# Kernel tuning notes

Hardware: AMD Instinct MI355X
Metric: run time of the kernel (lower is better)

Reference implementation:

```python
import jax, jax.numpy as jnp
import numpy as np

LN_EPS = 1e-5


def mlp_block(x, W, b, g, beta):
    # Linear -> LayerNorm -> ReLU  (MLP_Block)
    h = x @ W.T + b
    mu = jnp.mean(h, axis=-1, keepdims=True)
    var = jnp.mean((h - mu) ** 2, axis=-1, keepdims=True)
    h = (h - mu) / jnp.sqrt(var + LN_EPS) * g + beta
    return jax.nn.relu(h)


def interaction(a, bfeat, gW, gb, gg, gbt, pW, pb, pg, pbt, awg, abg, awp, abp):
    # Interaction_Estimator.forward(a, bfeat)
    g_align = mlp_block(a, gW, gb, gg, gbt)       # [B,L,D]
    p_align = mlp_block(bfeat, pW, pb, pg, pbt)    # [B,L,D]
    # atten[b,l,i,j] = g_align[b,l,i] * p_align[b,l,j]
    # geno_att[b,l,i] = sigmoid(sum_j atten[b,l,i,j]*awg[j] + abg)
    #               = sigmoid(g_align[b,l,i] * (p_align[b,l,:]\cdot awg) + abg)
    geno_att = jax.nn.sigmoid(g_align * jnp.einsum('bld,d->bl', p_align, awg)[..., None] + abg)
    # path_att[b,l,j] = sigmoid(sum_i atten[b,l,i,j]*awp[i] + abp)
    path_att = jax.nn.sigmoid(p_align * jnp.einsum('bld,d->bl', g_align, awp)[..., None] + abp)
    return p_align * path_att + g_align * geno_att


def setup_inputs() -> dict:
    B, L, D = 128, 16, 256
    key = jax.random.key(0)
    ks = iter(jax.random.split(key, 64))
    inp = {
        'gfeat': jax.random.normal(next(ks), (B, L, D), jnp.float32),
        'pfeat': jax.random.normal(next(ks), (B, L, D), jnp.float32),
    }

    def mlp_params(prefix):
        inp[prefix + '_W'] = jax.random.normal(next(ks), (D, D), jnp.float32) * 0.05
        inp[prefix + '_b'] = jnp.zeros((D,), jnp.float32)
        inp[prefix + '_g'] = jnp.ones((D,), jnp.float32)
        inp[prefix + '_beta'] = jnp.zeros((D,), jnp.float32)

    def atten_params(prefix):
        inp[prefix + 'w'] = jax.random.normal(next(ks), (D,), jnp.float32) * 0.05
        inp[prefix + 'b'] = jnp.zeros((), jnp.float32)

    mlp_params('gs')  # geno_spec
    mlp_params('ps')  # path_spec
    mlp_params('c_g'); mlp_params('c_p'); atten_params('c_ag'); atten_params('c_ap')  # common
    mlp_params('s_g'); mlp_params('s_p'); atten_params('s_ag'); atten_params('s_ap')  # synergy
    return inp


def reference(gfeat, pfeat,
              gs_W, gs_b, gs_g, gs_beta,
              ps_W, ps_b, ps_g, ps_beta,
              c_g_W, c_g_b, c_g_g, c_g_beta, c_p_W, c_p_b, c_p_g, c_p_beta, c_agw, c_agb, c_apw, c_apb,
              s_g_W, s_g_b, s_g_g, s_g_beta, s_p_W, s_p_b, s_p_g, s_p_beta, s_agw, s_agb, s_apw, s_apb):
    g_spec = mlp_block(gfeat, gs_W, gs_b, gs_g, gs_beta)
    p_spec = mlp_block(pfeat, ps_W, ps_b, ps_g, ps_beta)
    # NOTE: original calls encoder(pfeat, gfeat) (args swapped) -- kept faithful.
    common = interaction(pfeat, gfeat, c_g_W, c_g_b, c_g_g, c_g_beta,
                         c_p_W, c_p_b, c_p_g, c_p_beta, c_agw, c_agb, c_apw, c_apb)
    synergy = interaction(pfeat, gfeat, s_g_W, s_g_b, s_g_g, s_g_beta,
                          s_p_W, s_p_b, s_p_g, s_p_beta, s_agw, s_agb, s_apw, s_apb)
    return (common, synergy, g_spec, p_spec)
```

## Files before the change

### kernel.cpp

```cpp
#include <hip/hip_runtime.h>

typedef __attribute__((ext_vector_type(8))) short bf16x8;
typedef __attribute__((ext_vector_type(4))) float f32x4;
typedef unsigned short u16;
typedef unsigned int u32;

__device__ __forceinline__ u16 f2bf(float f) {
    u32 u = __builtin_bit_cast(u32, f);
    return (u16)((u + 0x7FFFu + ((u >> 16) & 1u)) >> 16);
}
__device__ __forceinline__ float sigm(float x) { return 1.f / (1.f + __expf(-x)); }
__device__ __forceinline__ float red16(float x) {
    x += __shfl_xor(x, 1, 64);
    x += __shfl_xor(x, 2, 64);
    x += __shfl_xor(x, 4, 64);
    x += __shfl_xor(x, 8, 64);
    return x;
}
__device__ __forceinline__ uint4 pack8(const float* s) {
    f32x4 v0 = *(const f32x4*)s;
    f32x4 v1 = *(const f32x4*)(s + 4);
    uint4 o;
    o.x = (u32)f2bf(v0.x) | ((u32)f2bf(v0.y) << 16);
    o.y = (u32)f2bf(v0.z) | ((u32)f2bf(v0.w) << 16);
    o.z = (u32)f2bf(v1.x) | ((u32)f2bf(v1.y) << 16);
    o.w = (u32)f2bf(v1.z) | ((u32)f2bf(v1.w) << 16);
    return o;
}

struct PrepArgs { const float* W[6]; const float* xg; const float* xp; u16* wf; u16* xf; };

__global__ __launch_bounds__(256) void prep_kernel(PrepArgs a) {
    int gid = blockIdx.x * 256 + threadIdx.x;
    if (gid < 49152) {
        int l = gid & 63, kk = (gid >> 6) & 7, nt = (gid >> 9) & 3,
            w = (gid >> 11) & 3, mlp = gid >> 13;
        int n = w * 64 + nt * 16 + (l & 15);
        int k0 = kk * 32 + (l >> 4) * 8;
        *(uint4*)(a.wf + (size_t)gid * 8) = pack8(a.W[mlp] + n * 256 + k0);
    } else if (gid < 49152 + 131072) {
        int r = gid - 49152;
        const float* x = (r >> 16) ? a.xp : a.xg;
        int q = r & 65535;
        int l = q & 63, kk = (q >> 6) & 7, mt = q >> 9;
        int row = mt * 16 + (l & 15);
        int k0 = kk * 32 + (l >> 4) * 8;
        *(uint4*)(a.xf + (size_t)r * 8) = pack8(x + row * 256 + k0);
    }
}

struct PairTask {
    const u16 *xfG, *xfP;
    const u16 *WG, *WP;
    const float *bG, *gmG, *beG;
    const float *bP, *gmP, *beP;
    const float *awG, *awP;
    const float *attbP, *attbG;
    float *outG, *outP;
    int interact;
};
struct FusedArgs { PairTask p[3]; };

__global__ __launch_bounds__(256) void fused_kernel(FusedArgs args) {
    __shared__ float red_s[2][16][4];
    __shared__ float red_q[2][16][4];
    __shared__ float red_d[2][16][4];

    int wg = blockIdx.x;
    int swz = (wg & 7) * 48 + (wg >> 3);
    int pair = swz >> 7;
    int mt = swz & 127;
    PairTask tk = args.p[pair];

    int tid = threadIdx.x;
    int wave = tid >> 6;
    int lane = tid & 63;
    int cq = lane & 15, rq = lane >> 4;

    float bb[2][4], gm[2][4], be[2][4], aw[2][4];
#pragma unroll
    for (int g = 0; g < 2; ++g)
#pragma unroll
        for (int nt = 0; nt < 4; ++nt) {
            int c = wave * 64 + nt * 16 + cq;
            bb[g][nt] = g ? tk.bP[c] : tk.bG[c];
            gm[g][nt] = g ? tk.gmP[c] : tk.gmG[c];
            be[g][nt] = g ? tk.beP[c] : tk.beG[c];
            aw[g][nt] = tk.interact ? (g ? tk.awP[c] : tk.awG[c]) : 0.f;
        }
    float battP = tk.interact ? *tk.attbP : 0.f;
    float battG = tk.interact ? *tk.attbG : 0.f;

    bf16x8 aF[2][8];
#pragma unroll
    for (int kk = 0; kk < 8; ++kk) {
        aF[0][kk] = *(const bf16x8*)(tk.xfG + ((size_t)(mt * 8 + kk) * 64 + lane) * 8);
        aF[1][kk] = *(const bf16x8*)(tk.xfP + ((size_t)(mt * 8 + kk) * 64 + lane) * 8);
    }

    f32x4 acc[2][4];
#pragma unroll
    for (int g = 0; g < 2; ++g)
#pragma unroll
        for (int nt = 0; nt < 4; ++nt) acc[g][nt] = (f32x4){0.f, 0.f, 0.f, 0.f};

    const u16* wb0 = tk.WG + (size_t)wave * 16384 + lane * 8;
    const u16* wb1 = tk.WP + (size_t)wave * 16384 + lane * 8;

#pragma unroll
    for (int kk = 0; kk < 8; ++kk) {
#pragma unroll
        for (int nt = 0; nt < 4; ++nt) {
            bf16x8 b0 = *(const bf16x8*)(wb0 + (size_t)(nt * 8 + kk) * 512);
            acc[0][nt] = __builtin_amdgcn_mfma_f32_16x16x32_bf16(aF[0][kk], b0, acc[0][nt], 0, 0, 0);
            bf16x8 b1 = *(const bf16x8*)(wb1 + (size_t)(nt * 8 + kk) * 512);
            acc[1][nt] = __builtin_amdgcn_mfma_f32_16x16x32_bf16(aF[1][kk], b1, acc[1][nt], 0, 0, 0);
        }
    }

    float v[2][4][4];
#pragma unroll
    for (int r = 0; r < 4; ++r) {
#pragma unroll
        for (int g = 0; g < 2; ++g) {
            float s = 0.f, q = 0.f;
#pragma unroll
            for (int nt = 0; nt < 4; ++nt) {
                float t = acc[g][nt][r] + bb[g][nt];
                v[g][nt][r] = t;
                s += t; q += t * t;
            }
            s = red16(s); q = red16(q);
            if (cq == 0) {
                red_s[g][rq * 4 + r][wave] = s;
                red_q[g][rq * 4 + r][wave] = q;
            }
        }
    }
    __syncthreads();

    float o[2][4][4];
#pragma unroll
    for (int r = 0; r < 4; ++r) {
        int row = rq * 4 + r;
#pragma unroll
        for (int g = 0; g < 2; ++g) {
            f32x4 s4 = *(const f32x4*)&red_s[g][row][0];
            f32x4 q4 = *(const f32x4*)&red_q[g][row][0];
            float s = s4.x + s4.y + s4.z + s4.w;
            float q = q4.x + q4.y + q4.z + q4.w;
            float mean = s * (1.f / 256.f);
            float var = q * (1.f / 256.f) - mean * mean;
            float rstd = rsqrtf(var + 1e-5f);
#pragma unroll
            for (int nt = 0; nt < 4; ++nt)
                o[g][nt][r] = fmaxf((v[g][nt][r] - mean) * rstd * gm[g][nt] + be[g][nt], 0.f);
        }
    }

    if (!tk.interact) {
#pragma unroll
        for (int r = 0; r < 4; ++r) {
            int grow = mt * 16 + rq * 4 + r;
#pragma unroll
            for (int nt = 0; nt < 4; ++nt) {
                int c = wave * 64 + nt * 16 + cq;
                tk.outG[(size_t)grow * 256 + c] = o[0][nt][r];
                tk.outP[(size_t)grow * 256 + c] = o[1][nt][r];
            }
        }
    } else {
#pragma unroll
        for (int r = 0; r < 4; ++r) {
            float dg = 0.f, dp = 0.f;
#pragma unroll
            for (int nt = 0; nt < 4; ++nt) {
                dg += o[0][nt][r] * aw[0][nt];
                dp += o[1][nt][r] * aw[1][nt];
            }
            dg = red16(dg); dp = red16(dp);
            if (cq == 0) {
                red_d[0][rq * 4 + r][wave] = dg;
                red_d[1][rq * 4 + r][wave] = dp;
            }
        }
        __syncthreads();
#pragma unroll
        for (int r = 0; r < 4; ++r) {
            int row = rq * 4 + r;
            f32x4 d4 = *(const f32x4*)&red_d[0][row][0];
            f32x4 e4 = *(const f32x4*)&red_d[1][row][0];
            float dG = d4.x + d4.y + d4.z + d4.w;
            float dP = e4.x + e4.y + e4.z + e4.w;
            int grow = mt * 16 + row;
#pragma unroll
            for (int nt = 0; nt < 4; ++nt) {
                int c = wave * 64 + nt * 16 + cq;
                float og = o[0][nt][r], op = o[1][nt][r];
                tk.outG[(size_t)grow * 256 + c] =
                    op * sigm(op * dG + battP) + og * sigm(og * dP + battG);
            }
        }
    }
}

extern "C" void kernel_launch(void* const* d_in, const int* in_sizes, int n_in,
                              void* d_out, int out_size, void* d_ws, size_t ws_size,
                              hipStream_t stream) {
    const float* gfeat = (const float*)d_in[0];
    const float* pfeat = (const float*)d_in[1];
    float* out = (float*)d_out;
    const size_t S = (size_t)2048 * 256;

    float* out_common = out + 0 * S;
    float* out_syn    = out + 1 * S;
    float* out_gspec  = out + 2 * S;
    float* out_pspec  = out + 3 * S;

    u16* wf = (u16*)d_ws;
    u16* xf = wf + 6 * 65536;
    u16* xf_g = xf;
    u16* xf_p = xf + 524288;

    PrepArgs pa;
    pa.W[0] = (const float*)d_in[2];
    pa.W[1] = (const float*)d_in[6];
    pa.W[2] = (const float*)d_in[10];
    pa.W[3] = (const float*)d_in[14];
    pa.W[4] = (const float*)d_in[22];
    pa.W[5] = (const float*)d_in[26];
    pa.xg = gfeat; pa.xp = pfeat;
    pa.wf = wf; pa.xf = xf;
    hipLaunchKernelGGL(prep_kernel, dim3(704), dim3(256), 0, stream, pa);

    FusedArgs fa;
    fa.p[0] = { xf_g, xf_p, wf + 0 * 65536, wf + 1 * 65536,
                (const float*)d_in[3], (const float*)d_in[4], (const float*)d_in[5],
                (const float*)d_in[7], (const float*)d_in[8], (const float*)d_in[9],
                nullptr, nullptr, nullptr, nullptr,
                out_gspec, out_pspec, 0 };
    fa.p[1] = { xf_p, xf_g, wf + 2 * 65536, wf + 3 * 65536,
                (const float*)d_in[11], (const float*)d_in[12], (const float*)d_in[13],
                (const float*)d_in[15], (const float*)d_in[16], (const float*)d_in[17],
                (const float*)d_in[20] , (const float*)d_in[18] ,
                (const float*)d_in[21] , (const float*)d_in[19] ,
                out_common, nullptr, 1 };
    fa.p[2] = { xf_p, xf_g, wf + 4 * 65536, wf + 5 * 65536,
                (const float*)d_in[23], (const float*)d_in[24], (const float*)d_in[25],
                (const float*)d_in[27], (const float*)d_in[28], (const float*)d_in[29],
                (const float*)d_in[32] , (const float*)d_in[30] ,
                (const float*)d_in[33] , (const float*)d_in[31] ,
                out_syn, nullptr, 1 };

    hipLaunchKernelGGL(fused_kernel, dim3(384), dim3(256), 0, stream, fa);
}
```

Baseline: 23.32 us.

## Replicate packed weights per XCD and software-pipeline loads in fused GEMM

The prep kernel now writes up to eight copies of the packed bf16 weights, one per XCD group (selected by wg&7), so each chiplet's blocks read weights from their own copy and hit their local L2 instead of contending across chiplets. The fused kernel no longer preloads all A fragments up front. It issues A and B fragment loads two K-steps ahead in a three-stage register ring, so memory latency overlaps the MFMA work. It also adds a launch-bounds occupancy hint of two blocks per SM. The cost is more prep work (eight times the weight conversion writes) and higher register pressure from the buffered fragments.

```diff
diff --git a/kernel.cpp b/kernel.cpp
--- a/kernel.cpp
+++ b/kernel.cpp
@@ -28,18 +28,25 @@
     return o;
 }
 
-struct PrepArgs { const float* W[6]; const float* xg; const float* xp; u16* wf; u16* xf; };
+struct PrepArgs {
+    const float* W[6]; const float* xg; const float* xp;
+    u16* wf; u16* xf; int nrep;
+};
 
 __global__ __launch_bounds__(256) void prep_kernel(PrepArgs a) {
-    int gid = blockIdx.x * 256 + threadIdx.x;
-    if (gid < 49152) {
+    int blk = blockIdx.x, tid = threadIdx.x;
+    int wblk = 192 * a.nrep;
+    if (blk < wblk) {
+        int rep = (a.nrep == 8) ? (blk & 7) : 0;
+        int gid = ((a.nrep == 8) ? (blk >> 3) : blk) * 256 + tid;
         int l = gid & 63, kk = (gid >> 6) & 7, nt = (gid >> 9) & 3,
             w = (gid >> 11) & 3, mlp = gid >> 13;
         int n = w * 64 + nt * 16 + (l & 15);
         int k0 = kk * 32 + (l >> 4) * 8;
-        *(uint4*)(a.wf + (size_t)gid * 8) = pack8(a.W[mlp] + n * 256 + k0);
-    } else if (gid < 49152 + 131072) {
-        int r = gid - 49152;
+        *(uint4*)(a.wf + ((size_t)rep * 49152 + gid) * 8) =
+            pack8(a.W[mlp] + n * 256 + k0);
+    } else {
+        int r = (blk - wblk) * 256 + tid;
         const float* x = (r >> 16) ? a.xp : a.xg;
         int q = r & 65535;
         int l = q & 63, kk = (q >> 6) & 7, mt = q >> 9;
@@ -51,7 +58,7 @@
 
 struct PairTask {
     const u16 *xfG, *xfP;
-    const u16 *WG, *WP;
+    int mlpG, mlpP;
     const float *bG, *gmG, *beG;
     const float *bP, *gmP, *beP;
     const float *awG, *awP;
@@ -59,9 +66,9 @@
     float *outG, *outP;
     int interact;
 };
-struct FusedArgs { PairTask p[3]; };
-
-__global__ __launch_bounds__(256) void fused_kernel(FusedArgs args) {
+struct FusedArgs { const u16* wf; int nrep; PairTask p[3]; };
+
+__global__ __launch_bounds__(256, 2) void fused_kernel(FusedArgs args) {
     __shared__ float red_s[2][16][4];
     __shared__ float red_q[2][16][4];
     __shared__ float red_d[2][16][4];
@@ -71,6 +78,7 @@
     int pair = swz >> 7;
     int mt = swz & 127;
     PairTask tk = args.p[pair];
+    int rep = (wg & 7) % args.nrep;
 
     int tid = threadIdx.x;
     int wave = tid >> 6;
@@ -91,32 +99,44 @@
     float battP = tk.interact ? *tk.attbP : 0.f;
     float battG = tk.interact ? *tk.attbG : 0.f;
 
-    bf16x8 aF[2][8];
+    f32x4 acc[2][4];
+#pragma unroll
+    for (int g = 0; g < 2; ++g)
+#pragma unroll
+        for (int nt = 0; nt < 4; ++nt) acc[g][nt] = (f32x4){0.f, 0.f, 0.f, 0.f};
+
+    const u16* xaG = tk.xfG + ((size_t)mt * 8 * 64 + lane) * 8;
+    const u16* xaP = tk.xfP + ((size_t)mt * 8 * 64 + lane) * 8;
+    const u16* wb0 = args.wf + ((size_t)rep * 6 + tk.mlpG) * 65536
+                             + (size_t)wave * 16384 + lane * 8;
+    const u16* wb1 = args.wf + ((size_t)rep * 6 + tk.mlpP) * 65536
+                             + (size_t)wave * 16384 + lane * 8;
+
+    bf16x8 bufA0[3], bufA1[3], bufB[3][8];
+#define ISSUE(KK, S)                                                       \
+    do {                                                                   \
+        bufA0[S] = *(const bf16x8*)(xaG + (KK) * 512);                     \
+        bufA1[S] = *(const bf16x8*)(xaP + (KK) * 512);                     \
+        _Pragma("unroll")                                                  \
+        for (int nt = 0; nt < 4; ++nt) {                                   \
+            bufB[S][nt]     = *(const bf16x8*)(wb0 + ((size_t)(nt * 8 + (KK)) * 512)); \
+            bufB[S][4 + nt] = *(const bf16x8*)(wb1 + ((size_t)(nt * 8 + (KK)) * 512)); \
+        }                                                                  \
+    } while (0)
+
+    ISSUE(0, 0);
+    ISSUE(1, 1);
 #pragma unroll
     for (int kk = 0; kk < 8; ++kk) {
-        aF[0][kk] = *(const bf16x8*)(tk.xfG + ((size_t)(mt * 8 + kk) * 64 + lane) * 8);
-        aF[1][kk] = *(const bf16x8*)(tk.xfP + ((size_t)(mt * 8 + kk) * 64 + lane) * 8);
-    }
-
-    f32x4 acc[2][4];
-#pragma unroll
-    for (int g = 0; g < 2; ++g)
-#pragma unroll
-        for (int nt = 0; nt < 4; ++nt) acc[g][nt] = (f32x4){0.f, 0.f, 0.f, 0.f};
-
-    const u16* wb0 = tk.WG + (size_t)wave * 16384 + lane * 8;
-    const u16* wb1 = tk.WP + (size_t)wave * 16384 + lane * 8;
-
-#pragma unroll
-    for (int kk = 0; kk < 8; ++kk) {
+        const int s = kk % 3;
+        if (kk + 2 < 8) ISSUE(kk + 2, (kk + 2) % 3);
 #pragma unroll
         for (int nt = 0; nt < 4; ++nt) {
-            bf16x8 b0 = *(const bf16x8*)(wb0 + (size_t)(nt * 8 + kk) * 512);
-            acc[0][nt] = __builtin_amdgcn_mfma_f32_16x16x32_bf16(aF[0][kk], b0, acc[0][nt], 0, 0, 0);
-            bf16x8 b1 = *(const bf16x8*)(wb1 + (size_t)(nt * 8 + kk) * 512);
-            acc[1][nt] = __builtin_amdgcn_mfma_f32_16x16x32_bf16(aF[1][kk], b1, acc[1][nt], 0, 0, 0);
-        }
-    }
+            acc[0][nt] = __builtin_amdgcn_mfma_f32_16x16x32_bf16(bufA0[s], bufB[s][nt], acc[0][nt], 0, 0, 0);
+            acc[1][nt] = __builtin_amdgcn_mfma_f32_16x16x32_bf16(bufA1[s], bufB[s][4 + nt], acc[1][nt], 0, 0, 0);
+        }
+    }
+#undef ISSUE
 
     float v[2][4][4];
 #pragma unroll
@@ -217,8 +237,10 @@
     float* out_gspec  = out + 2 * S;
     float* out_pspec  = out + 3 * S;
 
+    const size_t WF_REP = (size_t)49152 * 8;
+    int nrep = (ws_size >= (8 * WF_REP + 2 * 524288) * sizeof(u16) + 4096) ? 8 : 1;
     u16* wf = (u16*)d_ws;
-    u16* xf = wf + 6 * 65536;
+    u16* xf = wf + (size_t)nrep * WF_REP;
     u16* xf_g = xf;
     u16* xf_p = xf + 524288;
 
@@ -230,22 +252,23 @@
     pa.W[4] = (const float*)d_in[22];
     pa.W[5] = (const float*)d_in[26];
     pa.xg = gfeat; pa.xp = pfeat;
-    pa.wf = wf; pa.xf = xf;
-    hipLaunchKernelGGL(prep_kernel, dim3(704), dim3(256), 0, stream, pa);
+    pa.wf = wf; pa.xf = xf; pa.nrep = nrep;
+    hipLaunchKernelGGL(prep_kernel, dim3(192 * nrep + 512), dim3(256), 0, stream, pa);
 
     FusedArgs fa;
-    fa.p[0] = { xf_g, xf_p, wf + 0 * 65536, wf + 1 * 65536,
+    fa.wf = wf; fa.nrep = nrep;
+    fa.p[0] = { xf_g, xf_p, 0, 1,
                 (const float*)d_in[3], (const float*)d_in[4], (const float*)d_in[5],
                 (const float*)d_in[7], (const float*)d_in[8], (const float*)d_in[9],
                 nullptr, nullptr, nullptr, nullptr,
                 out_gspec, out_pspec, 0 };
-    fa.p[1] = { xf_p, xf_g, wf + 2 * 65536, wf + 3 * 65536,
+    fa.p[1] = { xf_p, xf_g, 2, 3,
                 (const float*)d_in[11], (const float*)d_in[12], (const float*)d_in[13],
                 (const float*)d_in[15], (const float*)d_in[16], (const float*)d_in[17],
                 (const float*)d_in[20] , (const float*)d_in[18] ,
                 (const float*)d_in[21] , (const float*)d_in[19] ,
                 out_common, nullptr, 1 };
-    fa.p[2] = { xf_p, xf_g, wf + 4 * 65536, wf + 5 * 65536,
+    fa.p[2] = { xf_p, xf_g, 4, 5,
                 (const float*)d_in[23], (const float*)d_in[24], (const float*)d_in[25],
                 (const float*)d_in[27], (const float*)d_in[28], (const float*)d_in[29],
                 (const float*)d_in[32] , (const float*)d_in[30] ,
```

Result: slower. 25.75 us (+10.4%).
